# Optimization experiments

Hardware: AMD Instinct MI355X
Metric: run time of the kernel (lower is better)

Reference implementation:

```python
import jax, jax.numpy as jnp
import numpy as np

B_, L, D_MODEL = 2, 4096, 2048
H, P, N, G, K = 32, 64, 128, 1, 4
EPS = 1e-5
INTER = H * P                      # 2048
CONV_DIM = INTER + 2 * G * N       # 2304
PROJ = INTER + CONV_DIM + H        # 4384


def setup_inputs() -> dict:
    key = jax.random.key(0)
    ks = jax.random.split(key, 5)
    hidden_states = jax.random.normal(ks[0], (B_, L, D_MODEL), jnp.float32)
    W_in = jax.random.normal(ks[1], (PROJ, D_MODEL), jnp.float32) * 0.02
    conv_w = jax.random.normal(ks[2], (CONV_DIM, K), jnp.float32) * 0.1
    conv_b = jnp.zeros((CONV_DIM,), jnp.float32)
    dt_bias = jnp.ones((H,), jnp.float32)
    A_log = jnp.log(jnp.arange(1, H + 1, dtype=jnp.float32))
    D_param = jnp.ones((H,), jnp.float32)
    norm_w = jnp.ones((INTER,), jnp.float32)
    W_out = jax.random.normal(ks[3], (D_MODEL, INTER), jnp.float32) * 0.02
    return dict(hidden_states=hidden_states, W_in=W_in, conv_w=conv_w, conv_b=conv_b,
                dt_bias=dt_bias, A_log=A_log, D_param=D_param, norm_w=norm_w, W_out=W_out)


def _silu(x):
    return x * jax.nn.sigmoid(x)


def _mamba2_mixer(hidden_states, W_in, conv_w, conv_b, dt_bias, A_log, D_param, norm_w, W_out):
    b, l, _ = hidden_states.shape
    # in_proj (no bias): [b, l, PROJ]
    proj = jnp.einsum('bld,pd->blp', hidden_states, W_in)
    gate = proj[..., :INTER]                     # [b, l, INTER]
    hBC = proj[..., INTER:INTER + CONV_DIM]      # [b, l, CONV_DIM]
    dt = proj[..., INTER + CONV_DIM:]            # [b, l, H]

    # depthwise causal conv1d + silu
    xc = jnp.transpose(hBC, (0, 2, 1))           # [b, C, l]
    conv = jax.lax.conv_general_dilated(
        xc, conv_w[:, None, :], window_strides=(1,), padding=[(K - 1, 0)],
        dimension_numbers=('NCH', 'OIH', 'NCH'), feature_group_count=CONV_DIM)
    hBC = _silu(jnp.transpose(conv + conv_b[None, :, None], (0, 2, 1)))  # [b, l, CONV_DIM]

    xs = hBC[..., :INTER].reshape(b, l, H, P)                 # [b, l, H, P]
    Bm = hBC[..., INTER:INTER + G * N].reshape(b, l, G, N)    # [b, l, G, N]
    Cm = hBC[..., INTER + G * N:].reshape(b, l, G, N)
    Bh = jnp.repeat(Bm, H // G, axis=2)                       # [b, l, H, N]
    Ch = jnp.repeat(Cm, H // G, axis=2)

    # dt softplus with bias; A = -exp(A_log)
    dt = jax.nn.softplus(dt + dt_bias)                        # [b, l, H]
    A = -jnp.exp(A_log)                                       # [H]
    dA = jnp.exp(dt * A)                                      # [b, l, H]

    # sequential selective scan over time (state h: [b, H, P, N])
    def step(h, inp):
        dA_t, dt_t, x_t, B_t, C_t = inp
        u = (dt_t[:, :, None] * x_t)[..., None] * B_t[:, :, None, :]   # [b,H,P,N]
        h = dA_t[:, :, None, None] * h + u
        y = jnp.einsum('bhpn,bhn->bhp', h, C_t)
        return h, y

    tm = lambda a: jnp.moveaxis(a, 1, 0)  # time-major
    h0 = jnp.zeros((b, H, P, N), hidden_states.dtype)
    _, ys = jax.lax.scan(step, h0, (tm(dA), tm(dt), tm(xs), tm(Bh), tm(Ch)))
    y = jnp.moveaxis(ys, 0, 1) + D_param[None, None, :, None] * xs   # [b, l, H, P]
    y = y.reshape(b, l, INTER)

    # gated RMSNorm (norm_before_gate=False, single group)
    g = y * _silu(gate)
    g = g * jax.lax.rsqrt(jnp.mean(g * g, axis=-1, keepdims=True) + EPS) * norm_w

    return jnp.einsum('bli,di->bld', g, W_out)   # [b, l, D_MODEL]


def reference(hidden_states, W_in, conv_w, conv_b, dt_bias, A_log, D_param, norm_w, W_out):
    return _mamba2_mixer(hidden_states, W_in, conv_w, conv_b, dt_bias, A_log, D_param, norm_w, W_out)
```

## Files before the change

### kernel.cpp

```cpp
#include <hip/hip_runtime.h>
#include <cstdint>
#include <cstddef>

#define B_        2
#define LSEQ      4096
#define DMODEL    2048
#define NH        32
#define PDIM      64
#define NSTATE    128
#define KCONV     4
#define INTER     2048
#define CONV_DIM  2304
#define HBCDT     2336
#define HBCDT_PAD 2432
#define ROWS      (B_*LSEQ)
#define NC        32
#define CLEN      (LSEQ/NC)

typedef unsigned short ushort_t;
typedef short bf16x8 __attribute__((ext_vector_type(8)));
typedef float f32x4 __attribute__((ext_vector_type(4)));

__device__ __forceinline__ float siluf(float x) {
  return x / (1.0f + __expf(-x));
}
__device__ __forceinline__ float bf2f(ushort_t u) {
  union { unsigned int i; float f; } v; v.i = ((unsigned int)u) << 16; return v.f;
}
__device__ __forceinline__ ushort_t f2bf(float f) {
  union { float f; unsigned int i; } v; v.f = f;
  unsigned int r = v.i + 0x7fff + ((v.i >> 16) & 1);
  return (ushort_t)(r >> 16);
}
__device__ __forceinline__ void async16(const void* g, void* l) {
  __builtin_amdgcn_global_load_lds(
      (const __attribute__((address_space(1))) unsigned int*)g,
      (__attribute__((address_space(3))) unsigned int*)l, 16, 0, 0);
}

__global__ __launch_bounds__(256) void cvt_f32_bf16(
    const float* __restrict__ src, ushort_t* __restrict__ dst, int n) {
  const int i = (blockIdx.x * 256 + threadIdx.x) * 4;
  if (i >= n) return;
  float4 v = *(const float4*)(src + i);
  ushort4 o; o.x = f2bf(v.x); o.y = f2bf(v.y); o.z = f2bf(v.z); o.w = f2bf(v.w);
  *(ushort4*)(dst + i) = o;
}

__global__ __launch_bounds__(256) void cvt_Wh(
    const float* __restrict__ W_in, ushort_t* __restrict__ dst) {
  const int i = (blockIdx.x * 256 + threadIdx.x) * 4;
  if (i >= HBCDT_PAD * DMODEL) return;
  const int r = i / DMODEL, c = i % DMODEL;
  ushort4 o;
  if (r < HBCDT) {
    float4 v = *(const float4*)(W_in + (size_t)(INTER + r) * DMODEL + c);
    o.x = f2bf(v.x); o.y = f2bf(v.y); o.z = f2bf(v.z); o.w = f2bf(v.w);
  } else {
    o.x = 0; o.y = 0; o.z = 0; o.w = 0;
  }
  *(ushort4*)(dst + i) = o;
}

template <bool OUT_BF16>
__global__ __launch_bounds__(256) void gemm_bf16_nt(
    const ushort_t* __restrict__ A, const ushort_t* __restrict__ B,
    void* __restrict__ C, int M, int N, int K, int ldc) {
  __shared__ __align__(16) char smem[16384];
  char* As = smem;
  char* Bs = smem + 8192;
  const int t    = threadIdx.x;
  const int lane = t & 63;
  const int wave = t >> 6;

  const int nwg = gridDim.x * gridDim.y;
  const int cpx = nwg >> 3;
  int bid = blockIdx.y * gridDim.x + blockIdx.x;
  bid = (bid & 7) * cpx + (bid >> 3);
  const int m0 = (bid / gridDim.x) * 128;
  const int n0 = (bid % gridDim.x) * 128;

  const int wm = wave & 1;
  const int wn = wave >> 1;

  f32x4 acc[4][4];
#pragma unroll
  for (int i = 0; i < 4; ++i)
#pragma unroll
    for (int j = 0; j < 4; ++j) {
      f32x4 z = {0.f, 0.f, 0.f, 0.f};
      acc[i][j] = z;
    }

  const int rowW   = wave * 32;
  const int lrow   = lane >> 2;
  const int lchunk = lane & 3;
  const ushort_t* Ag0 = A + (size_t)(m0 + rowW + lrow) * K + lchunk * 8;
  const ushort_t* Ag1 = Ag0 + (size_t)16 * K;
  const ushort_t* Bg0 = B + (size_t)(n0 + rowW + lrow) * K + lchunk * 8;
  const ushort_t* Bg1 = Bg0 + (size_t)16 * K;
  char* lA0 = As + rowW * 64;
  char* lA1 = As + (rowW + 16) * 64;
  char* lB0 = Bs + rowW * 64;
  char* lB1 = Bs + (rowW + 16) * 64;

  const int rA = wm * 64 + (lane & 15);
  const int rB = wn * 64 + (lane & 15);
  const int kq = (lane >> 4) * 16;

  for (int k0 = 0; k0 < K; k0 += 32) {
    async16(Ag0 + k0, lA0);
    async16(Ag1 + k0, lA1);
    async16(Bg0 + k0, lB0);
    async16(Bg1 + k0, lB1);
    __syncthreads();

    bf16x8 af[4], bfr[4];
#pragma unroll
    for (int i = 0; i < 4; ++i) {
      af[i]  = *(const bf16x8*)(As + (rA + i * 16) * 64 + kq);
      bfr[i] = *(const bf16x8*)(Bs + (rB + i * 16) * 64 + kq);
    }
#pragma unroll
    for (int i = 0; i < 4; ++i)
#pragma unroll
      for (int j = 0; j < 4; ++j)
        acc[i][j] = __builtin_amdgcn_mfma_f32_16x16x32_bf16(
            af[i], bfr[j], acc[i][j], 0, 0, 0);
    __syncthreads();
  }

  const int mbase = m0 + wm * 64 + (lane >> 4) * 4;
  const int nbase = n0 + wn * 64 + (lane & 15);
#pragma unroll
  for (int i = 0; i < 4; ++i)
#pragma unroll
    for (int j = 0; j < 4; ++j)
#pragma unroll
      for (int r = 0; r < 4; ++r) {
        const int m = mbase + i * 16 + r;
        const int n = nbase + j * 16;
        const float v = acc[i][j][r];
        if (OUT_BF16)
          ((ushort_t*)C)[(size_t)m * ldc + n] = f2bf(v);
        else
          ((float*)C)[(size_t)m * ldc + n] = v;
      }
}

__global__ __launch_bounds__(256) void conv_silu_kernel(
    const ushort_t* __restrict__ hbcdt, const float* __restrict__ conv_w,
    const float* __restrict__ conv_b, ushort_t* __restrict__ convo,
    ushort_t* __restrict__ BT_g) {
  const int idx = blockIdx.x * 256 + threadIdx.x;
  if (idx >= ROWS * CONV_DIM) return;
  const int c   = idx % CONV_DIM;
  const int row = idx / CONV_DIM;
  const int l   = row & (LSEQ - 1);
  float acc = conv_b[c];
  const float* w = conv_w + c * KCONV;
#pragma unroll
  for (int k = 0; k < KCONV; ++k) {
    const int tt = l + k - (KCONV - 1);
    if (tt >= 0)
      acc = fmaf(bf2f(hbcdt[(size_t)(row + k - (KCONV - 1)) * HBCDT_PAD + c]), w[k], acc);
  }
  const ushort_t v = f2bf(siluf(acc));
  convo[idx] = v;
  if (c >= INTER && c < INTER + NSTATE) {
    const int n   = c - INTER;
    const int bb  = row >> 12;
    const int cch = l >> 7;
    const int sl  = l & (CLEN - 1);
    BT_g[(((size_t)bb * NC + cch) * NSTATE + n) * CLEN + sl] = v;
  }
}

__global__ __launch_bounds__(256) void dtprep_kernel(
    const ushort_t* __restrict__ hbcdt, const float* __restrict__ dt_bias,
    float* __restrict__ dt_s) {
  const int idx = blockIdx.x * 256 + threadIdx.x;
  if (idx >= ROWS * NH) return;
  const int h   = idx & (NH - 1);
  const int row = idx >> 5;
  float x = bf2f(hbcdt[(size_t)row * HBCDT_PAD + CONV_DIM + h]) + dt_bias[h];
  dt_s[idx] = (x > 20.f) ? x : log1pf(__expf(x));
}

#define XLD 272
__global__ __launch_bounds__(256) void scan_state_kernel(
    const ushort_t* __restrict__ convo, const float* __restrict__ dt_s,
    const float* __restrict__ A_log, const ushort_t* __restrict__ BT_g,
    ushort_t* __restrict__ Sbuf, float* __restrict__ chunkA) {
  __shared__ __align__(16) char XwT[64 * XLD];
  __shared__ float dt_sh[CLEN];
  __shared__ float wgt[CLEN];

  const int blk = blockIdx.x;
  const int c   = blk & (NC - 1);
  const int h   = (blk >> 5) & 31;
  const int b   = blk >> 10;
  const int t   = threadIdx.x;
  const int lane = t & 63;
  const int wave = t >> 6;
  const size_t crow = (size_t)(b * LSEQ + c * CLEN);

  if (t < CLEN) dt_sh[t] = dt_s[(crow + t) * NH + h];
  __syncthreads();

  if (wave == 0) {
    const float a = __expf(A_log[h]);
    float v0 = -a * dt_sh[lane];
    float v1 = -a * dt_sh[lane + 64];
#pragma unroll
    for (int off = 1; off < 64; off <<= 1) {
      float u0 = __shfl_up(v0, off);
      float u1 = __shfl_up(v1, off);
      if (lane >= off) { v0 += u0; v1 += u1; }
    }
    const float tot0 = __shfl(v0, 63);
    const float La0  = v0;
    const float La1  = v1 + tot0;
    const float Lend = __shfl(v1, 63) + tot0;
    wgt[lane]      = dt_sh[lane]      * __expf(Lend - La0);
    wgt[lane + 64] = dt_sh[lane + 64] * __expf(Lend - La1);
    if (lane == 0) chunkA[(b * NH + h) * NC + c] = __expf(Lend);
  }
  __syncthreads();

  {
    const int p = lane;
    const int xcol = h * PDIM + p;
#pragma unroll
    for (int oct = 0; oct < 4; ++oct) {
      const int t0 = wave * 32 + oct * 8;
      unsigned int pk[4];
#pragma unroll
      for (int e = 0; e < 4; ++e) {
        const float f0 = bf2f(convo[(crow + t0 + 2*e)     * CONV_DIM + xcol]) * wgt[t0 + 2*e];
        const float f1 = bf2f(convo[(crow + t0 + 2*e + 1) * CONV_DIM + xcol]) * wgt[t0 + 2*e + 1];
        pk[e] = (unsigned int)f2bf(f0) | ((unsigned int)f2bf(f1) << 16);
      }
      *(uint4*)(XwT + p * XLD + t0 * 2) = make_uint4(pk[0], pk[1], pk[2], pk[3]);
    }
  }
  __syncthreads();

  f32x4 acc[8];
#pragma unroll
  for (int j = 0; j < 8; ++j) {
    f32x4 z = {0.f, 0.f, 0.f, 0.f};
    acc[j] = z;
  }
  const int rowA = wave * 16 + (lane & 15);
  const int koff = (lane >> 4) * 8;
  const ushort_t* Bt = BT_g + ((size_t)b * NC + c) * NSTATE * CLEN;
#pragma unroll
  for (int k0 = 0; k0 < 4; ++k0) {
    bf16x8 af = *(const bf16x8*)(XwT + rowA * XLD + (k0 * 32 + koff) * 2);
#pragma unroll
    for (int j = 0; j < 8; ++j) {
      bf16x8 bfx = *(const bf16x8*)(Bt + (size_t)(j * 16 + (lane & 15)) * CLEN + k0 * 32 + koff);
      acc[j] = __builtin_amdgcn_mfma_f32_16x16x32_bf16(af, bfx, acc[j], 0, 0, 0);
    }
  }

  ushort_t* Sb = Sbuf + (((size_t)b * NC + c) * NH + h) * (PDIM * NSTATE);
  const int prow = wave * 16 + (lane >> 4) * 4;
  const int ncol = lane & 15;
#pragma unroll
  for (int j = 0; j < 8; ++j)
#pragma unroll
    for (int r = 0; r < 4; ++r)
      Sb[(size_t)(prow + r) * NSTATE + j * 16 + ncol] = f2bf(acc[j][r]);
}

__global__ __launch_bounds__(256) void state_combine_kernel(
    ushort_t* __restrict__ Sbuf, const float* __restrict__ chunkA) {
  const int idx = blockIdx.x * 256 + threadIdx.x;
  const int nq = idx & 31;
  const int p  = (idx >> 5) & 63;
  const int h  = (idx >> 11) & 31;
  const int b  = (idx >> 16) & 1;
  const float* ca = chunkA + (b * NH + h) * NC;

  float s0 = 0.f, s1 = 0.f, s2 = 0.f, s3 = 0.f;
#pragma unroll 4
  for (int c = 0; c < NC; ++c) {
    const size_t off = ((((size_t)b * NC + c) * NH + h) * PDIM + p) * NSTATE + nq * 4;
    ushort4 loc = *(const ushort4*)(Sbuf + off);
    ushort4 o;
    o.x = f2bf(s0); o.y = f2bf(s1); o.z = f2bf(s2); o.w = f2bf(s3);
    *(ushort4*)(Sbuf + off) = o;
    const float a = ca[c];
    s0 = fmaf(a, s0, bf2f(loc.x));
    s1 = fmaf(a, s1, bf2f(loc.y));
    s2 = fmaf(a, s2, bf2f(loc.z));
    s3 = fmaf(a, s3, bf2f(loc.w));
  }
}

#define WLD 272
__global__ __launch_bounds__(256) void ssd_y_kernel(
    const ushort_t* __restrict__ convo, const float* __restrict__ dt_s,
    const float* __restrict__ A_log, const float* __restrict__ D_param,
    const ushort_t* __restrict__ Sbuf, ushort_t* __restrict__ ybuf) {
  __shared__ __align__(16) char XT[64 * 256];
  __shared__ __align__(16) char Wsh[128 * WLD];
  __shared__ float dt_sh[CLEN];
  __shared__ float La[CLEN];

  const int blk = blockIdx.x;
  const int c   = blk & (NC - 1);
  const int h   = (blk >> 5) & 31;
  const int b   = blk >> 10;
  const int t   = threadIdx.x;
  const int lane = t & 63;
  const int wave = t >> 6;

  const size_t crow = (size_t)(b * LSEQ + c * CLEN);

  {
    const int p = lane;
    const int xcol = h * PDIM + p;
#pragma unroll
    for (int oct = 0; oct < 4; ++oct) {
      const int tl0 = wave * 32 + oct * 8;
      unsigned int pk[4];
#pragma unroll
      for (int e = 0; e < 4; ++e) {
        ushort_t v0 = convo[(crow + tl0 + 2 * e) * CONV_DIM + xcol];
        ushort_t v1 = convo[(crow + tl0 + 2 * e + 1) * CONV_DIM + xcol];
        pk[e] = (unsigned int)v0 | ((unsigned int)v1 << 16);
      }
      const int tsw = tl0 ^ ((p & 7) << 3);
      *(uint4*)(XT + p * 256 + tsw * 2) = make_uint4(pk[0], pk[1], pk[2], pk[3]);
    }
  }
  if (t < CLEN) dt_sh[t] = dt_s[(crow + t) * NH + h];
  __syncthreads();

  if (wave == 0) {
    const float a = __expf(A_log[h]);
    float v0 = -a * dt_sh[lane];
    float v1 = -a * dt_sh[lane + 64];
#pragma unroll
    for (int off = 1; off < 64; off <<= 1) {
      float u0 = __shfl_up(v0, off);
      float u1 = __shfl_up(v1, off);
      if (lane >= off) { v0 += u0; v1 += u1; }
    }
    const float tot0 = __shfl(v0, 63);
    La[lane]      = v0;
    La[lane + 64] = v1 + tot0;
  }
  __syncthreads();

  const int wt = wave & 1;
  const int ws = wave >> 1;
  const bool active = !(wt == 0 && ws == 1);

  f32x4 g[4][4];
#pragma unroll
  for (int i = 0; i < 4; ++i)
#pragma unroll
    for (int j = 0; j < 4; ++j) {
      f32x4 z = {0.f, 0.f, 0.f, 0.f};
      g[i][j] = z;
    }

  if (active) {
    for (int k0 = 0; k0 < 4; ++k0) {
      const int koct = k0 * 32 + (lane >> 4) * 8;
      bf16x8 cf[4], bfg[4];
#pragma unroll
      for (int i = 0; i < 4; ++i) {
        const int tg = wt * 64 + i * 16 + (lane & 15);
        cf[i] = *(const bf16x8*)(convo + (crow + tg) * CONV_DIM + INTER + NSTATE + koct);
        const int sg = ws * 64 + i * 16 + (lane & 15);
        bfg[i] = *(const bf16x8*)(convo + (crow + sg) * CONV_DIM + INTER + koct);
      }
#pragma unroll
      for (int i = 0; i < 4; ++i)
#pragma unroll
        for (int j = 0; j < 4; ++j)
          g[i][j] = __builtin_amdgcn_mfma_f32_16x16x32_bf16(cf[i], bfg[j], g[i][j], 0, 0, 0);
    }
  }
#pragma unroll
  for (int i = 0; i < 4; ++i) {
    const int tbase = wt * 64 + i * 16 + ((lane >> 4) << 2);
    float Lat[4];
#pragma unroll
    for (int r = 0; r < 4; ++r) Lat[r] = La[tbase + r];
#pragma unroll
    for (int j = 0; j < 4; ++j) {
      const int sl  = ws * 64 + j * 16 + (lane & 15);
      const float Las = La[sl];
      const float dts = dt_sh[sl];
#pragma unroll
      for (int r = 0; r < 4; ++r) {
        const int tl = tbase + r;
        float val = 0.f;
        if (active && tl >= sl)
          val = g[i][j][r] * dts * __expf(Lat[r] - Las);
        *(ushort_t*)(Wsh + tl * WLD + sl * 2) = f2bf(val);
      }
    }
  }
  __syncthreads();

  const int yt = wave & 1;
  const int yp = wave >> 1;
  f32x4 acc[4][2];
#pragma unroll
  for (int i = 0; i < 4; ++i)
#pragma unroll
    for (int j = 0; j < 2; ++j) {
      f32x4 z = {0.f, 0.f, 0.f, 0.f};
      acc[i][j] = z;
    }

  const ushort_t* Sb = Sbuf + (((size_t)b * NC + c) * NH + h) * PDIM * NSTATE;

  for (int k0 = 0; k0 < 4; ++k0) {
    const int koct = k0 * 32 + (lane >> 4) * 8;
    bf16x8 af[4], sf[2];
#pragma unroll
    for (int i = 0; i < 4; ++i) {
      const int tg = yt * 64 + i * 16 + (lane & 15);
      af[i] = *(const bf16x8*)(convo + (crow + tg) * CONV_DIM + INTER + NSTATE + koct);
    }
#pragma unroll
    for (int j = 0; j < 2; ++j) {
      const int pr = yp * 32 + j * 16 + (lane & 15);
      sf[j] = *(const bf16x8*)(Sb + pr * NSTATE + koct);
    }
#pragma unroll
    for (int i = 0; i < 4; ++i)
#pragma unroll
      for (int j = 0; j < 2; ++j)
        acc[i][j] = __builtin_amdgcn_mfma_f32_16x16x32_bf16(af[i], sf[j], acc[i][j], 0, 0, 0);
  }
#pragma unroll
  for (int i = 0; i < 4; ++i) {
    const int tbase = yt * 64 + i * 16 + ((lane >> 4) << 2);
#pragma unroll
    for (int r = 0; r < 4; ++r) {
      const float e = __expf(La[tbase + r]);
#pragma unroll
      for (int j = 0; j < 2; ++j) acc[i][j][r] *= e;
    }
  }
  for (int k0 = 0; k0 < 4; ++k0) {
    const int koct = k0 * 32 + (lane >> 4) * 8;
    bf16x8 wf[4], xf[2];
#pragma unroll
    for (int i = 0; i < 4; ++i) {
      const int tl = yt * 64 + i * 16 + (lane & 15);
      wf[i] = *(const bf16x8*)(Wsh + tl * WLD + koct * 2);
    }
#pragma unroll
    for (int j = 0; j < 2; ++j) {
      const int pr  = yp * 32 + j * 16 + (lane & 15);
      const int tsw = koct ^ ((pr & 7) << 3);
      xf[j] = *(const bf16x8*)(XT + pr * 256 + tsw * 2);
    }
#pragma unroll
    for (int i = 0; i < 4; ++i)
#pragma unroll
      for (int j = 0; j < 2; ++j)
        acc[i][j] = __builtin_amdgcn_mfma_f32_16x16x32_bf16(wf[i], xf[j], acc[i][j], 0, 0, 0);
  }

  const float Dh = D_param[h];
#pragma unroll
  for (int i = 0; i < 4; ++i) {
    const int tbase = yt * 64 + i * 16 + ((lane >> 4) << 2);
#pragma unroll
    for (int j = 0; j < 2; ++j) {
      const int pr = yp * 32 + j * 16 + (lane & 15);
#pragma unroll
      for (int r = 0; r < 4; ++r) {
        const int tl  = tbase + r;
        const int tsw = tl ^ ((pr & 7) << 3);
        const float x = bf2f(*(const ushort_t*)(XT + pr * 256 + tsw * 2));
        ybuf[(crow + tl) * INTER + h * PDIM + pr] = f2bf(acc[i][j][r] + Dh * x);
      }
    }
  }
}

__global__ __launch_bounds__(256) void gated_rmsnorm_kernel(
    ushort_t* __restrict__ y, const ushort_t* __restrict__ gate,
    const float* __restrict__ norm_w) {
  const int row = blockIdx.x;
  ushort_t* yr = y + (size_t)row * INTER;
  const ushort_t* gr = gate + (size_t)row * INTER;
  const int t  = threadIdx.x;
  const int i0 = t * 8;

  ushort4 ya = *(const ushort4*)(yr + i0);
  ushort4 yb = *(const ushort4*)(yr + i0 + 4);
  ushort4 ga = *(const ushort4*)(gr + i0);
  ushort4 gb = *(const ushort4*)(gr + i0 + 4);

  float g[8];
  g[0] = bf2f(ya.x) * siluf(bf2f(ga.x));
  g[1] = bf2f(ya.y) * siluf(bf2f(ga.y));
  g[2] = bf2f(ya.z) * siluf(bf2f(ga.z));
  g[3] = bf2f(ya.w) * siluf(bf2f(ga.w));
  g[4] = bf2f(yb.x) * siluf(bf2f(gb.x));
  g[5] = bf2f(yb.y) * siluf(bf2f(gb.y));
  g[6] = bf2f(yb.z) * siluf(bf2f(gb.z));
  g[7] = bf2f(yb.w) * siluf(bf2f(gb.w));

  float ss = 0.f;
#pragma unroll
  for (int i = 0; i < 8; ++i) ss += g[i] * g[i];

  ss += __shfl_xor(ss, 32);
  ss += __shfl_xor(ss, 16);
  ss += __shfl_xor(ss, 8);
  ss += __shfl_xor(ss, 4);
  ss += __shfl_xor(ss, 2);
  ss += __shfl_xor(ss, 1);

  __shared__ float red[4];
  if ((t & 63) == 0) red[t >> 6] = ss;
  __syncthreads();
  const float tot = red[0] + red[1] + red[2] + red[3];
  const float scale = rsqrtf(tot * (1.0f / INTER) + 1e-5f);

  ushort4 o0, o1;
  o0.x = f2bf(g[0] * scale * norm_w[i0 + 0]);
  o0.y = f2bf(g[1] * scale * norm_w[i0 + 1]);
  o0.z = f2bf(g[2] * scale * norm_w[i0 + 2]);
  o0.w = f2bf(g[3] * scale * norm_w[i0 + 3]);
  o1.x = f2bf(g[4] * scale * norm_w[i0 + 4]);
  o1.y = f2bf(g[5] * scale * norm_w[i0 + 5]);
  o1.z = f2bf(g[6] * scale * norm_w[i0 + 6]);
  o1.w = f2bf(g[7] * scale * norm_w[i0 + 7]);
  *(ushort4*)(yr + i0)     = o0;
  *(ushort4*)(yr + i0 + 4) = o1;
}

extern "C" void kernel_launch(void* const* d_in, const int* in_sizes, int n_in,
                              void* d_out, int out_size, void* d_ws, size_t ws_size,
                              hipStream_t stream) {
  const float* hs      = (const float*)d_in[0];
  const float* W_in    = (const float*)d_in[1];
  const float* conv_w  = (const float*)d_in[2];
  const float* conv_b  = (const float*)d_in[3];
  const float* dt_bias = (const float*)d_in[4];
  const float* A_log   = (const float*)d_in[5];
  const float* D_param = (const float*)d_in[6];
  const float* norm_w  = (const float*)d_in[7];
  const float* W_out   = (const float*)d_in[8];
  float* out = (float*)d_out;

  char* ws = (char*)d_ws;
  size_t off = 0;
  ushort_t* hbcdt_bf = (ushort_t*)(ws + off); off += (size_t)ROWS * HBCDT_PAD * 2;
  ushort_t* convo    = (ushort_t*)(ws + off); off += (size_t)ROWS * CONV_DIM * 2;
  float*    dt_s     = (float*)(ws + off);    off += (size_t)ROWS * NH * 4;
  ushort_t* Wh_bf    = (ushort_t*)(ws + off); off += (size_t)HBCDT_PAD * DMODEL * 2;
  ushort_t* Wg_bf    = (ushort_t*)(ws + off); off += (size_t)DMODEL * DMODEL * 2;
  ushort_t* Wout_bf  = (ushort_t*)(ws + off); off += (size_t)DMODEL * DMODEL * 2;
  float*    chunkA   = (float*)(ws + off);    off += (size_t)B_ * NH * NC * 4;
  ushort_t* BT_g     = (ushort_t*)(ws + off); off += (size_t)B_ * NC * NSTATE * CLEN * 2;
  ushort_t* ybuf_bf  = hbcdt_bf;

  char* outc = (char*)d_out;
  ushort_t* gate_bf = (ushort_t*)outc;
  ushort_t* hs_bf   = (ushort_t*)(outc + (size_t)ROWS * INTER * 2);
  ushort_t* Sbuf    = hs_bf;

  cvt_f32_bf16<<<(ROWS * DMODEL / 4 + 255) / 256, 256, 0, stream>>>(
      hs, hs_bf, ROWS * DMODEL);
  cvt_Wh<<<(HBCDT_PAD * DMODEL / 4 + 255) / 256, 256, 0, stream>>>(W_in, Wh_bf);
  cvt_f32_bf16<<<(DMODEL * DMODEL / 4 + 255) / 256, 256, 0, stream>>>(
      W_in, Wg_bf, DMODEL * DMODEL);
  cvt_f32_bf16<<<(DMODEL * DMODEL / 4 + 255) / 256, 256, 0, stream>>>(
      W_out, Wout_bf, DMODEL * DMODEL);

  {
    dim3 grid(HBCDT_PAD / 128, ROWS / 128);
    gemm_bf16_nt<true><<<grid, 256, 0, stream>>>(
        hs_bf, Wh_bf, hbcdt_bf, ROWS, HBCDT_PAD, DMODEL, HBCDT_PAD);
  }
  {
    dim3 grid(INTER / 128, ROWS / 128);
    gemm_bf16_nt<true><<<grid, 256, 0, stream>>>(
        hs_bf, Wg_bf, gate_bf, ROWS, INTER, DMODEL, INTER);
  }
  conv_silu_kernel<<<(ROWS * CONV_DIM + 255) / 256, 256, 0, stream>>>(
      hbcdt_bf, conv_w, conv_b, convo, BT_g);
  dtprep_kernel<<<(ROWS * NH + 255) / 256, 256, 0, stream>>>(
      hbcdt_bf, dt_bias, dt_s);
  scan_state_kernel<<<B_ * NH * NC, 256, 0, stream>>>(
      convo, dt_s, A_log, BT_g, Sbuf, chunkA);
  state_combine_kernel<<<(B_ * NH * PDIM * (NSTATE / 4)) / 256, 256, 0, stream>>>(
      Sbuf, chunkA);
  ssd_y_kernel<<<B_ * NH * NC, 256, 0, stream>>>(
      convo, dt_s, A_log, D_param, Sbuf, ybuf_bf);
  gated_rmsnorm_kernel<<<ROWS, 256, 0, stream>>>(ybuf_bf, gate_bf, norm_w);
  {
    dim3 grid(DMODEL / 128, ROWS / 128);
    gemm_bf16_nt<false><<<grid, 256, 0, stream>>>(
        ybuf_bf, Wout_bf, out, ROWS, DMODEL, INTER, DMODEL);
  }
}
```

Baseline: 711.6 us.

## Replace 128x128 GEMM with double-buffered 256x256 tile GEMM using swizzled LDS

Replaces the simple 128x128, single-buffered bf16 GEMM with a 256x256 tile, 512-thread kernel. It double-buffers 64-wide K slabs in 128KB of LDS, uses an XOR-swizzled LDS layout, and interleaves async global-to-LDS loads with MFMA phases, using explicit barriers and setprio. The goal is more data reuse per tile, hidden load latency and fewer LDS bank conflicts in all three projection GEMMs. The W_h weight is padded to 2560 rows so its tiles divide evenly, with stores masked past the valid columns. K is hard-coded to 2048, and the large LDS footprint limits how many workgroups fit per CU.

```diff
diff --git a/kernel.cpp b/kernel.cpp
--- a/kernel.cpp
+++ b/kernel.cpp
@@ -13,6 +13,7 @@
 #define CONV_DIM  2304
 #define HBCDT     2336
 #define HBCDT_PAD 2432
+#define WH_ROWS   2560
 #define ROWS      (B_*LSEQ)
 #define NC        32
 #define CLEN      (LSEQ/NC)
@@ -50,7 +51,7 @@
 __global__ __launch_bounds__(256) void cvt_Wh(
     const float* __restrict__ W_in, ushort_t* __restrict__ dst) {
   const int i = (blockIdx.x * 256 + threadIdx.x) * 4;
-  if (i >= HBCDT_PAD * DMODEL) return;
+  if (i >= WH_ROWS * DMODEL) return;
   const int r = i / DMODEL, c = i % DMODEL;
   ushort4 o;
   if (r < HBCDT) {
@@ -62,89 +63,148 @@
   *(ushort4*)(dst + i) = o;
 }
 
-template <bool OUT_BF16>
-__global__ __launch_bounds__(256) void gemm_bf16_nt(
+#define STAGE_A(CN, H, KTT) do {                                              \
+    async16(Ast + (size_t)((H) * 128) * 2048 + (KTT) * 64,                    \
+            smem_ + (CN) + (H) * 16384 + wave * 1024);                        \
+    async16(Ast + (size_t)((H) * 128 + 64) * 2048 + (KTT) * 64,               \
+            smem_ + (CN) + (H) * 16384 + 8192 + wave * 1024);                 \
+  } while (0)
+
+#define STAGE_B(CN, H, KTT) do {                                              \
+    async16(Bst + (size_t)((H) * 128) * 2048 + (KTT) * 64,                    \
+            smem_ + 65536 + (CN) + (H) * 16384 + wave * 1024);                \
+    async16(Bst + (size_t)((H) * 128 + 64) * 2048 + (KTT) * 64,               \
+            smem_ + 65536 + (CN) + (H) * 16384 + 8192 + wave * 1024);         \
+  } while (0)
+
+#define LDA(DST, CB, MH) do {                                                 \
+    const char* ab_ = smem_ + (CB) + aro;                                     \
+    _Pragma("unroll") for (int mi_ = 0; mi_ < 4; ++mi_) {                     \
+      DST[mi_][0] = *(const bf16x8*)(ab_ + (MH) * 8192 + mi_ * 2048 + g0);    \
+      DST[mi_][1] = *(const bf16x8*)(ab_ + (MH) * 8192 + mi_ * 2048 + g1);    \
+    }                                                                         \
+  } while (0)
+
+#define LDB(DST, CB, NHH) do {                                                \
+    const char* bb_ = smem_ + 65536 + (CB) + bro;                             \
+    _Pragma("unroll") for (int ni_ = 0; ni_ < 2; ++ni_) {                     \
+      DST[ni_][0] = *(const bf16x8*)(bb_ + (NHH) * 4096 + ni_ * 2048 + g0);   \
+      DST[ni_][1] = *(const bf16x8*)(bb_ + (NHH) * 4096 + ni_ * 2048 + g1);   \
+    }                                                                         \
+  } while (0)
+
+#define MFMAQ(MH, NHH, AF, BF)                                                \
+  _Pragma("unroll") for (int mi_ = 0; mi_ < 4; ++mi_)                         \
+  _Pragma("unroll") for (int ni_ = 0; ni_ < 2; ++ni_) {                       \
+    f32x4& c_ = acc[(MH) * 4 + mi_][(NHH) * 2 + ni_];                         \
+    c_ = __builtin_amdgcn_mfma_f32_16x16x32_bf16(AF[mi_][0], BF[ni_][0], c_, 0, 0, 0); \
+    c_ = __builtin_amdgcn_mfma_f32_16x16x32_bf16(AF[mi_][1], BF[ni_][1], c_, 0, 0, 0); \
+  }
+
+#define PH(X) do {                                                            \
+    __builtin_amdgcn_s_barrier();                                             \
+    asm volatile("s_waitcnt lgkmcnt(0)" ::: "memory");                        \
+    __builtin_amdgcn_sched_barrier(0);                                        \
+    __builtin_amdgcn_s_setprio(1);                                            \
+    X;                                                                        \
+    __builtin_amdgcn_s_setprio(0);                                            \
+    __builtin_amdgcn_s_barrier();                                             \
+  } while (0)
+
+#define GROUP_TAIL(X) do {                                                    \
+    __builtin_amdgcn_s_barrier();                                             \
+    asm volatile("s_waitcnt lgkmcnt(0)" ::: "memory");                        \
+    __builtin_amdgcn_sched_barrier(0);                                        \
+    __builtin_amdgcn_s_setprio(1);                                            \
+    X;                                                                        \
+    __builtin_amdgcn_s_setprio(0);                                            \
+    asm volatile("s_waitcnt vmcnt(0)" ::: "memory");                          \
+    __builtin_amdgcn_s_barrier();                                             \
+  } while (0)
+
+template <bool OUT_BF16, int NTN, int NVALID, int LDC>
+__global__ __launch_bounds__(512, 2) void gemm256_nt(
     const ushort_t* __restrict__ A, const ushort_t* __restrict__ B,
-    void* __restrict__ C, int M, int N, int K, int ldc) {
-  __shared__ __align__(16) char smem[16384];
-  char* As = smem;
-  char* Bs = smem + 8192;
+    void* __restrict__ C) {
+  __shared__ __align__(16) char smem_[131072];
   const int t    = threadIdx.x;
   const int lane = t & 63;
   const int wave = t >> 6;
-
-  const int nwg = gridDim.x * gridDim.y;
-  const int cpx = nwg >> 3;
-  int bid = blockIdx.y * gridDim.x + blockIdx.x;
-  bid = (bid & 7) * cpx + (bid >> 3);
-  const int m0 = (bid / gridDim.x) * 128;
-  const int n0 = (bid % gridDim.x) * 128;
-
-  const int wm = wave & 1;
-  const int wn = wave >> 1;
-
-  f32x4 acc[4][4];
-#pragma unroll
-  for (int i = 0; i < 4; ++i)
+  const int wm   = wave >> 2;
+  const int wn   = wave & 3;
+
+  constexpr int NWG = NTN * 32;
+  int bid = blockIdx.y * NTN + blockIdx.x;
+  bid = (bid & 7) * (NWG >> 3) + (bid >> 3);
+  const int m0 = (bid / NTN) * 256;
+  const int n0 = (bid % NTN) * 256;
+
+  const int srow = wave * 8 + (lane >> 3);
+  const int scol = ((lane & 7) ^ (lane >> 3)) * 8;
+  const ushort_t* Ast = A + (size_t)(m0 + srow) * 2048 + scol;
+  const ushort_t* Bst = B + (size_t)(n0 + srow) * 2048 + scol;
+
+  const int aro = (wm * 128 + (lane & 15)) * 128;
+  const int bro = (wn * 64 + (lane & 15)) * 128;
+  const int g0  = ((lane >> 4) ^ (lane & 7)) * 16;
+  const int g1  = (((lane >> 4) + 4) ^ (lane & 7)) * 16;
+
+  f32x4 acc[8][4];
+#pragma unroll
+  for (int i = 0; i < 8; ++i)
 #pragma unroll
     for (int j = 0; j < 4; ++j) {
       f32x4 z = {0.f, 0.f, 0.f, 0.f};
       acc[i][j] = z;
     }
-
-  const int rowW   = wave * 32;
-  const int lrow   = lane >> 2;
-  const int lchunk = lane & 3;
-  const ushort_t* Ag0 = A + (size_t)(m0 + rowW + lrow) * K + lchunk * 8;
-  const ushort_t* Ag1 = Ag0 + (size_t)16 * K;
-  const ushort_t* Bg0 = B + (size_t)(n0 + rowW + lrow) * K + lchunk * 8;
-  const ushort_t* Bg1 = Bg0 + (size_t)16 * K;
-  char* lA0 = As + rowW * 64;
-  char* lA1 = As + (rowW + 16) * 64;
-  char* lB0 = Bs + rowW * 64;
-  char* lB1 = Bs + (rowW + 16) * 64;
-
-  const int rA = wm * 64 + (lane & 15);
-  const int rB = wn * 64 + (lane & 15);
-  const int kq = (lane >> 4) * 16;
-
-  for (int k0 = 0; k0 < K; k0 += 32) {
-    async16(Ag0 + k0, lA0);
-    async16(Ag1 + k0, lA1);
-    async16(Bg0 + k0, lB0);
-    async16(Bg1 + k0, lB1);
-    __syncthreads();
-
-    bf16x8 af[4], bfr[4];
-#pragma unroll
-    for (int i = 0; i < 4; ++i) {
-      af[i]  = *(const bf16x8*)(As + (rA + i * 16) * 64 + kq);
-      bfr[i] = *(const bf16x8*)(Bs + (rB + i * 16) * 64 + kq);
-    }
-#pragma unroll
-    for (int i = 0; i < 4; ++i)
-#pragma unroll
-      for (int j = 0; j < 4; ++j)
-        acc[i][j] = __builtin_amdgcn_mfma_f32_16x16x32_bf16(
-            af[i], bfr[j], acc[i][j], 0, 0, 0);
-    __syncthreads();
-  }
-
-  const int mbase = m0 + wm * 64 + (lane >> 4) * 4;
-  const int nbase = n0 + wn * 64 + (lane & 15);
-#pragma unroll
-  for (int i = 0; i < 4; ++i)
-#pragma unroll
-    for (int j = 0; j < 4; ++j)
+  bf16x8 af[4][2], bq0[2][2], bq1[2][2];
+
+  STAGE_A(0, 0, 0); STAGE_A(0, 1, 0);
+  STAGE_B(0, 0, 0); STAGE_B(0, 1, 0);
+  asm volatile("s_waitcnt vmcnt(0)" ::: "memory");
+  __builtin_amdgcn_s_barrier();
+
+  constexpr int NT = 2048 / 64;
+  for (int kt = 0; kt < NT; kt += 2) {
+    STAGE_A(32768, 0, kt + 1); STAGE_A(32768, 1, kt + 1);
+    LDA(af, 0, 0); LDB(bq0, 0, 0);
+    PH(MFMAQ(0, 0, af, bq0));
+    STAGE_B(32768, 0, kt + 1); STAGE_B(32768, 1, kt + 1);
+    LDB(bq1, 0, 1);
+    PH(MFMAQ(0, 1, af, bq1));
+    LDA(af, 0, 1); LDB(bq0, 0, 0);
+    PH(MFMAQ(1, 0, af, bq0));
+    LDB(bq1, 0, 1);
+    GROUP_TAIL(MFMAQ(1, 1, af, bq1));
+    const bool more = (kt + 2) < NT;
+    if (more) { STAGE_A(0, 0, kt + 2); STAGE_A(0, 1, kt + 2); }
+    LDA(af, 32768, 0); LDB(bq0, 32768, 0);
+    PH(MFMAQ(0, 0, af, bq0));
+    if (more) { STAGE_B(0, 0, kt + 2); STAGE_B(0, 1, kt + 2); }
+    LDB(bq1, 32768, 1);
+    PH(MFMAQ(0, 1, af, bq1));
+    LDA(af, 32768, 1); LDB(bq0, 32768, 0);
+    PH(MFMAQ(1, 0, af, bq0));
+    LDB(bq1, 32768, 1);
+    GROUP_TAIL(MFMAQ(1, 1, af, bq1));
+  }
+
+  const int mb = m0 + wm * 128 + (lane >> 4) * 4;
+  const int nb = n0 + wn * 64 + (lane & 15);
+#pragma unroll
+  for (int mq = 0; mq < 8; ++mq)
+#pragma unroll
+    for (int nq = 0; nq < 4; ++nq)
 #pragma unroll
       for (int r = 0; r < 4; ++r) {
-        const int m = mbase + i * 16 + r;
-        const int n = nbase + j * 16;
-        const float v = acc[i][j][r];
-        if (OUT_BF16)
-          ((ushort_t*)C)[(size_t)m * ldc + n] = f2bf(v);
-        else
-          ((float*)C)[(size_t)m * ldc + n] = v;
+        const int m = mb + mq * 16 + r;
+        const int n = nb + nq * 16;
+        if (n < NVALID) {
+          if (OUT_BF16)
+            ((ushort_t*)C)[(size_t)m * LDC + n] = f2bf(acc[mq][nq][r]);
+          else
+            ((float*)C)[(size_t)m * LDC + n] = acc[mq][nq][r];
+        }
       }
 }
 
@@ -564,7 +624,7 @@
   ushort_t* hbcdt_bf = (ushort_t*)(ws + off); off += (size_t)ROWS * HBCDT_PAD * 2;
   ushort_t* convo    = (ushort_t*)(ws + off); off += (size_t)ROWS * CONV_DIM * 2;
   float*    dt_s     = (float*)(ws + off);    off += (size_t)ROWS * NH * 4;
-  ushort_t* Wh_bf    = (ushort_t*)(ws + off); off += (size_t)HBCDT_PAD * DMODEL * 2;
+  ushort_t* Wh_bf    = (ushort_t*)(ws + off); off += (size_t)WH_ROWS * DMODEL * 2;
   ushort_t* Wg_bf    = (ushort_t*)(ws + off); off += (size_t)DMODEL * DMODEL * 2;
   ushort_t* Wout_bf  = (ushort_t*)(ws + off); off += (size_t)DMODEL * DMODEL * 2;
   float*    chunkA   = (float*)(ws + off);    off += (size_t)B_ * NH * NC * 4;
@@ -578,22 +638,16 @@
 
   cvt_f32_bf16<<<(ROWS * DMODEL / 4 + 255) / 256, 256, 0, stream>>>(
       hs, hs_bf, ROWS * DMODEL);
-  cvt_Wh<<<(HBCDT_PAD * DMODEL / 4 + 255) / 256, 256, 0, stream>>>(W_in, Wh_bf);
+  cvt_Wh<<<(WH_ROWS * DMODEL / 4 + 255) / 256, 256, 0, stream>>>(W_in, Wh_bf);
   cvt_f32_bf16<<<(DMODEL * DMODEL / 4 + 255) / 256, 256, 0, stream>>>(
       W_in, Wg_bf, DMODEL * DMODEL);
   cvt_f32_bf16<<<(DMODEL * DMODEL / 4 + 255) / 256, 256, 0, stream>>>(
       W_out, Wout_bf, DMODEL * DMODEL);
 
-  {
-    dim3 grid(HBCDT_PAD / 128, ROWS / 128);
-    gemm_bf16_nt<true><<<grid, 256, 0, stream>>>(
-        hs_bf, Wh_bf, hbcdt_bf, ROWS, HBCDT_PAD, DMODEL, HBCDT_PAD);
-  }
-  {
-    dim3 grid(INTER / 128, ROWS / 128);
-    gemm_bf16_nt<true><<<grid, 256, 0, stream>>>(
-        hs_bf, Wg_bf, gate_bf, ROWS, INTER, DMODEL, INTER);
-  }
+  gemm256_nt<true, 10, HBCDT_PAD, HBCDT_PAD><<<dim3(10, 32), 512, 0, stream>>>(
+      hs_bf, Wh_bf, hbcdt_bf);
+  gemm256_nt<true, 8, INTER, INTER><<<dim3(8, 32), 512, 0, stream>>>(
+      hs_bf, Wg_bf, gate_bf);
   conv_silu_kernel<<<(ROWS * CONV_DIM + 255) / 256, 256, 0, stream>>>(
       hbcdt_bf, conv_w, conv_b, convo, BT_g);
   dtprep_kernel<<<(ROWS * NH + 255) / 256, 256, 0, stream>>>(
@@ -605,9 +659,6 @@
   ssd_y_kernel<<<B_ * NH * NC, 256, 0, stream>>>(
       convo, dt_s, A_log, D_param, Sbuf, ybuf_bf);
   gated_rmsnorm_kernel<<<ROWS, 256, 0, stream>>>(ybuf_bf, gate_bf, norm_w);
-  {
-    dim3 grid(DMODEL / 128, ROWS / 128);
-    gemm_bf16_nt<false><<<grid, 256, 0, stream>>>(
-        ybuf_bf, Wout_bf, out, ROWS, DMODEL, INTER, DMODEL);
-  }
-}
+  gemm256_nt<false, 8, DMODEL, DMODEL><<<dim3(8, 32), 512, 0, stream>>>(
+      ybuf_bf, Wout_bf, out);
+}
```

Result: faster. 640.6 us (-10.0%).
